# Performance work log

Measured on AMD Instinct MI355X. Metric: run time of the kernel, lower is better.

## Reference

```python
import jax, jax.numpy as jnp
import numpy as np

STEPS = 8  # number of scaling-and-squaring steps


def _identity_grid(D, H, W, dtype):
    # (D, H, W, 3) voxel-coordinate identity transformation
    z = jnp.arange(D, dtype=dtype)
    y = jnp.arange(H, dtype=dtype)
    x = jnp.arange(W, dtype=dtype)
    return jnp.stack(jnp.meshgrid(z, y, x, indexing='ij'), axis=-1)


def _pull_wrap(v, phi):
    """Trilinear sampling of field v at voxel coords phi with circular ('dft') bound.

    v:   (B, D, H, W, 3) vector field (values)
    phi: (B, D, H, W, 3) sampling coordinates in voxel space (z, y, x order)
    """
    B, D, H, W, C = v.shape
    f = jnp.floor(phi)
    w1 = phi - f          # weight of the +1 corner
    w0 = 1.0 - w1
    i0 = f.astype(jnp.int32)
    dims = jnp.array([D, H, W], dtype=jnp.int32)
    i0 = jnp.mod(i0, dims)          # wrap (dft) boundary
    i1 = jnp.mod(i0 + 1, dims)
    zs, ys, xs = (i0[..., 0], i1[..., 0]), (i0[..., 1], i1[..., 1]), (i0[..., 2], i1[..., 2])
    wzs, wys, wxs = (w0[..., 0], w1[..., 0]), (w0[..., 1], w1[..., 1]), (w0[..., 2], w1[..., 2])
    vflat = v.reshape(B, D * H * W, C)
    out = jnp.zeros_like(v)
    for a in range(2):
        for b in range(2):
            for c in range(2):
                lin = (zs[a] * H + ys[b]) * W + xs[c]              # (B, D, H, W)
                vals = jnp.take_along_axis(vflat, lin.reshape(B, -1, 1), axis=1)
                vals = vals.reshape(B, D, H, W, C)
                out = out + (wzs[a] * wys[b] * wxs[c])[..., None] * vals
    return out


def setup_inputs() -> dict:
    key = jax.random.key(0)
    velocity = jax.random.normal(key, (2, 128, 128, 128, 3), dtype=jnp.float32)
    return {"velocity": velocity}


def reference(velocity):
    # Scaling and squaring: v <- v/2^K; repeat K times: v <- v + v o (id + v)
    B, D, H, W, C = velocity.shape
    grid = _identity_grid(D, H, W, velocity.dtype)[None]  # (1, D, H, W, 3)
    v = velocity / (2.0 ** STEPS)
    for _ in range(STEPS):
        v = v + _pull_wrap(v, grid + v)
    # displacement=False -> return transformation field id + displacement
    return grid + v
```

## Files before the change

### kernel.cpp

```cpp
#include <hip/hip_runtime.h>
#include <hip/hip_fp16.h>


#define DHW   (128 * 128 * 128)
#define NVOX  (2 * DHW)
#define RW    129

#if defined(__has_builtin)
#  if __has_builtin(__builtin_amdgcn_global_load_lds)
#    define HAVE_ASYNC 1
#  endif
#endif
#ifndef HAVE_ASYNC
#  define HAVE_ASYNC 0
#endif

#if HAVE_ASYNC
#define ASYNC_DW(lptr, gptr)                                            \
    __builtin_amdgcn_global_load_lds(                                   \
        (__attribute__((address_space(1))) void*)(gptr),                \
        (__attribute__((address_space(3))) void*)(lptr), 4, 0, 0)
#else
#define ASYNC_DW(lptr, gptr)  (*(lptr) = *(gptr))
#endif

__device__ __forceinline__ __half2 bc_h2(unsigned u) {
    return *reinterpret_cast<__half2*>(&u);
}

__device__ __forceinline__ void acc_cell(uint2 c, float w,
                                         float& az, float& ay, float& ax) {
    __half2 c0 = bc_h2(c.x), c1 = bc_h2(c.y);
    az = fmaf(w, __low2float(c0),  az);
    ay = fmaf(w, __high2float(c0), ay);
    ax = fmaf(w, __low2float(c1),  ax);
}

template <bool IN_F32, int H, int BX, int BZ, int NB, bool PAD_OUT>
__global__ __launch_bounds__(512) void sq_sten_async(
    const float* __restrict__ velf,
    const uint2* __restrict__ fin,
    uint2* __restrict__ fout)
{
    constexpr int LBX = (BX == 64) ? 6 : 5;
    constexpr int TX = BX + 2 * H, TY = 8 + 2 * H, TZ = BZ + 2 * H;
    constexpr int TS = TX * TY * TZ;
    constexpr int DWS = TS * 2;
    constexpr int NP  = (DWS + 511) / 512;
    constexpr int PF  = (TS + 511) / 512;
    constexpr int VPT = (BX * BZ) / 64;
    constexpr int NXB = 128 / BX, LNX = 7 - LBX;
    static_assert(2 * TS * 8 <= 64 * 1024, "dbuf exceeds 64KB static LDS");
    static_assert(128 % (BZ * NB) == 0 && 128 / (BZ * NB) == 8, "z grouping");
    __shared__ uint2 lds[2][TS];

    int t = (int)threadIdx.x;
    int b = (int)blockIdx.x;
    int X = (b & (NXB - 1)) << LBX;
    int b2 = b >> LNX;
    int Y = (b2 & 15) << 3;
    int b3 = b2 >> 4;
    int Z0 = (b3 & 7) * (BZ * NB);
    int batch = b3 >> 3;
    int bb21 = batch << 21;

    unsigned sxy[NP];
    unsigned szzp[(NP + 3) / 4];
    if (!IN_F32) {
#pragma unroll
        for (int q = 0; q < (NP + 3) / 4; ++q) szzp[q] = 0;
#pragma unroll
        for (int p = 0; p < NP; ++p) {
            int idx = t + p * 512;
            if (idx < DWS) {
                int cell = idx >> 1, half = idx & 1;
                int xx = cell % TX;
                int rem = cell / TX;
                int yy = rem % TY, zz = rem / TY;
                int gx = (X - H + xx) & 127;
                int gy = (Y - H + yy) & 127;
                sxy[p] = (unsigned)(((((gy << 7) | gx)) << 1) | half);
                szzp[p >> 2] |= (unsigned)zz << ((p & 3) * 8);
            } else {
                sxy[p] = 0;
            }
        }
    }

    const unsigned* fdw = (const unsigned*)fin;

#define STAGE_ASYNC(ZB, BUF)                                            \
    { unsigned* ldw = (unsigned*)(BUF);                                 \
      _Pragma("unroll")                                                 \
      for (int p = 0; p < NP; ++p) {                                    \
          int idx = t + p * 512;                                        \
          if (idx < DWS) {                                              \
              int zz = (int)((szzp[p >> 2] >> ((p & 3) * 8)) & 255u);   \
              int gz = ((ZB) - H + zz) & 127;                           \
              ASYNC_DW(ldw + idx,                                       \
                       fdw + (bb21 << 1) + (gz << 15) + (int)sxy[p]);   \
          }                                                             \
      } }

#define STAGE_F32(ZB, BUF)                                              \
    { _Pragma("unroll")                                                 \
      for (int p = 0; p < PF; ++p) {                                    \
          int idx = t + p * 512;                                        \
          if (idx < TS) {                                               \
              int xx = idx % TX;                                        \
              int rem = idx / TX;                                       \
              int yy = rem % TY, zz = rem / TY;                         \
              int gx = (X - H + xx) & 127;                              \
              int gy = (Y - H + yy) & 127;                              \
              int gz = ((ZB) - H + zz) & 127;                           \
              size_t a = (size_t)((batch << 21) | (gz << 14) |          \
                                  (gy << 7) | gx) * 3;                  \
              const float s = 1.0f / 256.0f;                            \
              __half2 q0 = __floats2half2_rn(velf[a] * s,               \
                                             velf[a + 1] * s);          \
              __half2 q1 = __floats2half2_rn(velf[a + 2] * s, 0.0f);    \
              uint2 cc;                                                 \
              cc.x = *reinterpret_cast<unsigned*>(&q0);                 \
              cc.y = *reinterpret_cast<unsigned*>(&q1);                 \
              (BUF)[idx] = cc;                                          \
          }                                                             \
      } }

    if (IN_F32) { STAGE_F32(Z0, lds[0]) }
    else        { STAGE_ASYNC(Z0, lds[0]) }
    __syncthreads();

    int lx = t & (BX - 1);
    int ly = (t >> LBX) & 7;
    int lz0 = (t >> (LBX + 3)) * VPT;

    for (int i = 0; i < NB; ++i) {
        int Z = Z0 + i * BZ;
        const uint2* tile = IN_F32 ? lds[0] : lds[i & 1];

        if (!IN_F32 && i + 1 < NB) { STAGE_ASYNC(Z + BZ, lds[(i + 1) & 1]) }

        uint2 sd[VPT];
#pragma unroll
        for (int v = 0; v < VPT; ++v) {
            int lz = lz0 + v;
            int cidx = ((lz + H) * TY + (ly + H)) * TX + (lx + H);
            uint2 c = tile[cidx];
            __half2 c0 = bc_h2(c.x), c1 = bc_h2(c.y);
            float vz = __low2float(c0), vy = __high2float(c0), vx = __low2float(c1);

            float pz = (float)(Z + lz) + vz;
            float py = (float)(Y + ly) + vy;
            float px = (float)(X + lx) + vx;
            float fz = floorf(pz), fy = floorf(py), fx = floorf(px);
            float wz1 = pz - fz, wy1 = py - fy, wx1 = px - fx;
            float wz0 = 1.0f - wz1, wy0 = 1.0f - wy1, wx0 = 1.0f - wx1;

            int izl = (int)fz - Z + H;
            int iyl = (int)fy - Y + H;
            int ixl = (int)fx - X + H;

            float wzy00 = wz0 * wy0, wzy01 = wz0 * wy1;
            float wzy10 = wz1 * wy0, wzy11 = wz1 * wy1;

            float az = 0.0f, ay = 0.0f, ax = 0.0f;
            int i00 = (izl * TY + iyl) * TX + ixl;
            int i01 = i00 + TX;
            int i10 = i00 + TY * TX;
            int i11 = i10 + TX;

            acc_cell(tile[i00],     wzy00 * wx0, az, ay, ax);
            acc_cell(tile[i00 + 1], wzy00 * wx1, az, ay, ax);
            acc_cell(tile[i01],     wzy01 * wx0, az, ay, ax);
            acc_cell(tile[i01 + 1], wzy01 * wx1, az, ay, ax);
            acc_cell(tile[i10],     wzy10 * wx0, az, ay, ax);
            acc_cell(tile[i10 + 1], wzy10 * wx1, az, ay, ax);
            acc_cell(tile[i11],     wzy11 * wx0, az, ay, ax);
            acc_cell(tile[i11 + 1], wzy11 * wx1, az, ay, ax);

            __half2 p0 = __floats2half2_rn(vz + az, vy + ay);
            __half2 p1 = __floats2half2_rn(vx + ax, 0.0f);
            sd[v].x = *reinterpret_cast<unsigned*>(&p0);
            sd[v].y = *reinterpret_cast<unsigned*>(&p1);
        }

#pragma unroll
        for (int v = 0; v < VPT; ++v) {
            int lz = lz0 + v;
            int z_ = Z + lz, y_ = Y + ly, x_ = X + lx;
            if (PAD_OUT) {
                int rS = (batch << 14) + (z_ << 7) + y_;
                int pidx = (rS << 7) + rS + x_;
                fout[pidx] = sd[v];
                if (x_ == 0) fout[pidx + 128] = sd[v];
            } else {
                fout[bb21 | (z_ << 14) | (y_ << 7) | x_] = sd[v];
            }
        }

        if (i + 1 < NB) {
            __syncthreads();
            if (IN_F32) { STAGE_F32(Z + BZ, lds[0]) __syncthreads(); }
        }
    }
#undef STAGE_ASYNC
#undef STAGE_F32
}

__device__ __forceinline__ void acc_pair(uint4 g, float wl, float wr,
                                         float& az, float& ay, float& ax) {
    __half2 h0 = bc_h2(g.x);
    __half2 h1 = bc_h2(g.y);
    __half2 h2 = bc_h2(g.z);
    __half2 h3 = bc_h2(g.w);
    az += wl * __low2float(h0)  + wr * __low2float(h2);
    ay += wl * __high2float(h0) + wr * __high2float(h2);
    ax += wl * __low2float(h1)  + wr * __low2float(h3);
}

template <bool IN_F32, bool OUT_F32>
__global__ __launch_bounds__(1024) void sq_step_p(
    const void* __restrict__ vin_, void* __restrict__ vout_)
{
    const float* vinf = (const float*)vin_;
    const uint2* vinh = (const uint2*)vin_;

    int t = (int)threadIdx.x;
    int b = (int)blockIdx.x;
    int x = ((b & 1) << 6) | (t & 63);
    int y = (((b >> 1) & 31) << 2) | ((t >> 6) & 3);
    int z = (((b >> 6) & 31) << 2) | (t >> 8);
    int batch = b >> 11;

    const float s = IN_F32 ? (1.0f / 256.0f) : 1.0f;

    int bbr = batch << 14;
    int r   = bbr + (z << 7) + y;

    float vz, vy, vx;
    if (IN_F32) {
        size_t base = ((size_t)(batch << 21) + (z << 14) + (y << 7) + x) * 3;
        vz = vinf[base + 0] * s;
        vy = vinf[base + 1] * s;
        vx = vinf[base + 2] * s;
    } else {
        uint2 c = vinh[(r << 7) + r + x];
        __half2 c0 = bc_h2(c.x), c1 = bc_h2(c.y);
        vz = __low2float(c0); vy = __high2float(c0); vx = __low2float(c1);
    }

    float pz = (float)z + vz, py = (float)y + vy, px = (float)x + vx;
    float fz = floorf(pz), fy = floorf(py), fx = floorf(px);
    float wz1 = pz - fz, wy1 = py - fy, wx1 = px - fx;
    float wz0 = 1.0f - wz1, wy0 = 1.0f - wy1, wx0 = 1.0f - wx1;

    int iz0 = ((int)fz) & 127, iy0 = ((int)fy) & 127, ix0 = ((int)fx) & 127;
    int iz1 = (iz0 + 1) & 127, iy1 = (iy0 + 1) & 127;

    float wzy00 = wz0 * wy0, wzy01 = wz0 * wy1;
    float wzy10 = wz1 * wy0, wzy11 = wz1 * wy1;

    float az = 0.0f, ay = 0.0f, ax = 0.0f;

    if (IN_F32) {
        int bb  = batch << 21;
        int ix1 = (ix0 + 1) & 127;
        int zo0 = bb + (iz0 << 14), zo1 = bb + (iz1 << 14);
        int yo0 = iy0 << 7, yo1 = iy1 << 7;
#define CORNER(ZO, YO, IX, WW)                                          \
        {                                                               \
            size_t a = (size_t)((ZO) + (YO) + (IX)) * 3;                \
            float w = (WW);                                             \
            az += w * (vinf[a] * s);                                    \
            ay += w * (vinf[a + 1] * s);                                \
            ax += w * (vinf[a + 2] * s);                                \
        }
        CORNER(zo0, yo0, ix0, wzy00 * wx0)
        CORNER(zo0, yo0, ix1, wzy00 * wx1)
        CORNER(zo0, yo1, ix0, wzy01 * wx0)
        CORNER(zo0, yo1, ix1, wzy01 * wx1)
        CORNER(zo1, yo0, ix0, wzy10 * wx0)
        CORNER(zo1, yo0, ix1, wzy10 * wx1)
        CORNER(zo1, yo1, ix0, wzy11 * wx0)
        CORNER(zo1, yo1, ix1, wzy11 * wx1)
#undef CORNER
    } else {
        int r00 = bbr + (iz0 << 7) + iy0;
        int r01 = bbr + (iz0 << 7) + iy1;
        int r10 = bbr + (iz1 << 7) + iy0;
        int r11 = bbr + (iz1 << 7) + iy1;
        uint4 g00 = *(const uint4*)(vinh + (r00 << 7) + r00 + ix0);
        uint4 g01 = *(const uint4*)(vinh + (r01 << 7) + r01 + ix0);
        uint4 g10 = *(const uint4*)(vinh + (r10 << 7) + r10 + ix0);
        uint4 g11 = *(const uint4*)(vinh + (r11 << 7) + r11 + ix0);
        acc_pair(g00, wzy00 * wx0, wzy00 * wx1, az, ay, ax);
        acc_pair(g01, wzy01 * wx0, wzy01 * wx1, az, ay, ax);
        acc_pair(g10, wzy10 * wx0, wzy10 * wx1, az, ay, ax);
        acc_pair(g11, wzy11 * wx0, wzy11 * wx1, az, ay, ax);
    }

    float oz = vz + az;
    float oy = vy + ay;
    float ox = vx + ax;

    if (OUT_F32) {
        float* voutf = (float*)vout_;
        size_t base = ((size_t)(batch << 21) + (z << 14) + (y << 7) + x) * 3;
        voutf[base + 0] = oz + (float)z;
        voutf[base + 1] = oy + (float)y;
        voutf[base + 2] = ox + (float)x;
    } else {
        __half2 p0 = __floats2half2_rn(oz, oy);
        __half2 p1 = __floats2half2_rn(ox, 0.0f);
        uint2 sd;
        sd.x = *reinterpret_cast<unsigned*>(&p0);
        sd.y = *reinterpret_cast<unsigned*>(&p1);
        uint2* vouth = (uint2*)vout_;
        int pidx = (r << 7) + r + x;
        vouth[pidx] = sd;
        if (x == 0) vouth[pidx + 128] = sd;
    }
}

extern "C" void kernel_launch(void* const* d_in, const int* in_sizes, int n_in,
                              void* d_out, int out_size, void* d_ws, size_t ws_size,
                              hipStream_t stream) {
    const float* vel = (const float*)d_in[0];
    float* out = (float*)d_out;

    const size_t UB = (size_t)NVOX * 8;
    const size_t PB = (size_t)2 * 128 * 128 * RW * 8;

    dim3 pblock(512);
    dim3 pgrid1(512);
    dim3 pgrid2(1024);
    dim3 ggrid(NVOX / 1024), gblock(1024);

    if (ws_size >= 2 * UB + PB) {
        uint2* U0 = (uint2*)d_ws;
        uint2* U1 = (uint2*)((char*)d_ws + UB);
        uint2* P  = (uint2*)((char*)d_ws + 2 * UB);

        sq_sten_async<true,  1, 64, 4, 4, false><<<pgrid1, pblock, 0, stream>>>(vel, nullptr, U0);
        sq_sten_async<false, 1, 64, 4, 4, false><<<pgrid1, pblock, 0, stream>>>(nullptr, U0, U1);
        sq_sten_async<false, 1, 64, 4, 4, false><<<pgrid1, pblock, 0, stream>>>(nullptr, U1, U0);
        sq_sten_async<false, 1, 64, 4, 4, false><<<pgrid1, pblock, 0, stream>>>(nullptr, U0, U1);
        sq_sten_async<false, 1, 64, 4, 4, false><<<pgrid1, pblock, 0, stream>>>(nullptr, U1, U0);
        sq_sten_async<false, 1, 64, 4, 4, false><<<pgrid1, pblock, 0, stream>>>(nullptr, U0, U1);
        sq_sten_async<false, 2, 32, 4, 4, true ><<<pgrid2, pblock, 0, stream>>>(nullptr, U1, P);
        sq_step_p<false, true ><<<ggrid, gblock, 0, stream>>>(P, out);
    } else {
        void* ws = d_ws;
        sq_step_p<true,  false><<<ggrid, gblock, 0, stream>>>(vel, ws);
        sq_step_p<false, false><<<ggrid, gblock, 0, stream>>>(ws,  out);
        sq_step_p<false, false><<<ggrid, gblock, 0, stream>>>(out, ws);
        sq_step_p<false, false><<<ggrid, gblock, 0, stream>>>(ws,  out);
        sq_step_p<false, false><<<ggrid, gblock, 0, stream>>>(out, ws);
        sq_step_p<false, false><<<ggrid, gblock, 0, stream>>>(ws,  out);
        sq_step_p<false, false><<<ggrid, gblock, 0, stream>>>(out, ws);
        sq_step_p<false, true ><<<ggrid, gblock, 0, stream>>>(ws,  out);
    }
}
```

Baseline: 276.8 us.

## Unroll brick pipeline with fine-grained vmcnt waits and split first-step kernel

The async stencil kernel is split into a dedicated fp32-input first-step kernel and an fp16 DMA kernel. The DMA kernel's four z-bricks are fully unrolled with two named LDS buffers, and each brick writes its outputs inline instead of buffering them. Per-brick __syncthreads is replaced by an explicit s_waitcnt vmcnt(N) that still lets the last brick's global stores be in flight, plus an lgkmcnt wait, sched barriers and s_barrier. The goal is to stop blocking on outstanding stores at each brick boundary and to remove the template branching. The hand-written vmcnt literal assumes a fixed ordering of memory ops, which is fragile if the compiler reorders them.

```diff
diff --git a/kernel.cpp b/kernel.cpp
--- a/kernel.cpp
+++ b/kernel.cpp
@@ -15,15 +15,6 @@
 #  define HAVE_ASYNC 0
 #endif
 
-#if HAVE_ASYNC
-#define ASYNC_DW(lptr, gptr)                                            \
-    __builtin_amdgcn_global_load_lds(                                   \
-        (__attribute__((address_space(1))) void*)(gptr),                \
-        (__attribute__((address_space(3))) void*)(lptr), 4, 0, 0)
-#else
-#define ASYNC_DW(lptr, gptr)  (*(lptr) = *(gptr))
-#endif
-
 __device__ __forceinline__ __half2 bc_h2(unsigned u) {
     return *reinterpret_cast<__half2*>(&u);
 }
@@ -36,23 +27,22 @@
     ax = fmaf(w, __low2float(c1),  ax);
 }
 
-template <bool IN_F32, int H, int BX, int BZ, int NB, bool PAD_OUT>
-__global__ __launch_bounds__(512) void sq_sten_async(
-    const float* __restrict__ velf,
-    const uint2* __restrict__ fin,
-    uint2* __restrict__ fout)
+template <int H, int BX, int BZ, bool PAD_OUT>
+__global__ __launch_bounds__(512) void sq_sten_dma(
+    const uint2* __restrict__ fin, uint2* __restrict__ fout)
 {
     constexpr int LBX = (BX == 64) ? 6 : 5;
+    constexpr int NB = 4;
     constexpr int TX = BX + 2 * H, TY = 8 + 2 * H, TZ = BZ + 2 * H;
     constexpr int TS = TX * TY * TZ;
     constexpr int DWS = TS * 2;
     constexpr int NP  = (DWS + 511) / 512;
-    constexpr int PF  = (TS + 511) / 512;
     constexpr int VPT = (BX * BZ) / 64;
     constexpr int NXB = 128 / BX, LNX = 7 - LBX;
     static_assert(2 * TS * 8 <= 64 * 1024, "dbuf exceeds 64KB static LDS");
-    static_assert(128 % (BZ * NB) == 0 && 128 / (BZ * NB) == 8, "z grouping");
-    __shared__ uint2 lds[2][TS];
+    static_assert(VPT == 4 || VPT == 2, "vmcnt literal needs 4 or 2");
+    __shared__ uint2 bufA[TS];
+    __shared__ uint2 bufB[TS];
 
     int t = (int)threadIdx.x;
     int b = (int)blockIdx.x;
@@ -66,30 +56,37 @@
 
     unsigned sxy[NP];
     unsigned szzp[(NP + 3) / 4];
-    if (!IN_F32) {
 #pragma unroll
-        for (int q = 0; q < (NP + 3) / 4; ++q) szzp[q] = 0;
+    for (int q = 0; q < (NP + 3) / 4; ++q) szzp[q] = 0;
 #pragma unroll
-        for (int p = 0; p < NP; ++p) {
-            int idx = t + p * 512;
-            if (idx < DWS) {
-                int cell = idx >> 1, half = idx & 1;
-                int xx = cell % TX;
-                int rem = cell / TX;
-                int yy = rem % TY, zz = rem / TY;
-                int gx = (X - H + xx) & 127;
-                int gy = (Y - H + yy) & 127;
-                sxy[p] = (unsigned)(((((gy << 7) | gx)) << 1) | half);
-                szzp[p >> 2] |= (unsigned)zz << ((p & 3) * 8);
-            } else {
-                sxy[p] = 0;
-            }
+    for (int p = 0; p < NP; ++p) {
+        int idx = t + p * 512;
+        if (idx < DWS) {
+            int cell = idx >> 1, half = idx & 1;
+            int xx = cell % TX;
+            int rem = cell / TX;
+            int yy = rem % TY, zz = rem / TY;
+            int gx = (X - H + xx) & 127;
+            int gy = (Y - H + yy) & 127;
+            sxy[p] = (unsigned)((((gy << 7) | gx) << 1) | half);
+            szzp[p >> 2] |= (unsigned)zz << ((p & 3) * 8);
+        } else {
+            sxy[p] = 0;
         }
     }
 
     const unsigned* fdw = (const unsigned*)fin;
 
-#define STAGE_ASYNC(ZB, BUF)                                            \
+#if HAVE_ASYNC
+#define ASYNC_DW(lptr, gptr)                                            \
+    __builtin_amdgcn_global_load_lds(                                   \
+        (const __attribute__((address_space(1))) unsigned*)(gptr),      \
+        (__attribute__((address_space(3))) unsigned*)(lptr), 4, 0, 0)
+#else
+#define ASYNC_DW(lptr, gptr)  (*(lptr) = *(gptr))
+#endif
+
+#define STAGE(ZB, BUF)                                                  \
     { unsigned* ldw = (unsigned*)(BUF);                                 \
       _Pragma("unroll")                                                 \
       for (int p = 0; p < NP; ++p) {                                    \
@@ -100,75 +97,164 @@
               ASYNC_DW(ldw + idx,                                       \
                        fdw + (bb21 << 1) + (gz << 15) + (int)sxy[p]);   \
           }                                                             \
-      } }
-
-#define STAGE_F32(ZB, BUF)                                              \
-    { _Pragma("unroll")                                                 \
-      for (int p = 0; p < PF; ++p) {                                    \
-          int idx = t + p * 512;                                        \
-          if (idx < TS) {                                               \
-              int xx = idx % TX;                                        \
-              int rem = idx / TX;                                       \
-              int yy = rem % TY, zz = rem / TY;                         \
-              int gx = (X - H + xx) & 127;                              \
-              int gy = (Y - H + yy) & 127;                              \
-              int gz = ((ZB) - H + zz) & 127;                           \
-              size_t a = (size_t)((batch << 21) | (gz << 14) |          \
-                                  (gy << 7) | gx) * 3;                  \
-              const float s = 1.0f / 256.0f;                            \
-              __half2 q0 = __floats2half2_rn(velf[a] * s,               \
-                                             velf[a + 1] * s);          \
-              __half2 q1 = __floats2half2_rn(velf[a + 2] * s, 0.0f);    \
-              uint2 cc;                                                 \
-              cc.x = *reinterpret_cast<unsigned*>(&q0);                 \
-              cc.y = *reinterpret_cast<unsigned*>(&q1);                 \
-              (BUF)[idx] = cc;                                          \
-          }                                                             \
-      } }
-
-    if (IN_F32) { STAGE_F32(Z0, lds[0]) }
-    else        { STAGE_ASYNC(Z0, lds[0]) }
-    __syncthreads();
+      }                                                                 \
+      __builtin_amdgcn_sched_barrier(0); }
 
     int lx = t & (BX - 1);
     int ly = (t >> LBX) & 7;
     int lz0 = (t >> (LBX + 3)) * VPT;
 
-    for (int i = 0; i < NB; ++i) {
+#define COMPUTE(TILE, Z)                                                \
+    { _Pragma("unroll")                                                 \
+      for (int v = 0; v < VPT; ++v) {                                   \
+          int lz = lz0 + v;                                             \
+          int cidx = ((lz + H) * TY + (ly + H)) * TX + (lx + H);        \
+          uint2 c = (TILE)[cidx];                                       \
+          __half2 c0 = bc_h2(c.x), c1 = bc_h2(c.y);                     \
+          float vz = __low2float(c0), vy = __high2float(c0);            \
+          float vx = __low2float(c1);                                   \
+          float pz = (float)((Z) + lz) + vz;                            \
+          float py = (float)(Y + ly) + vy;                              \
+          float px = (float)(X + lx) + vx;                              \
+          float fz = floorf(pz), fy = floorf(py), fx = floorf(px);      \
+          float wz1 = pz - fz, wy1 = py - fy, wx1 = px - fx;            \
+          float wz0 = 1.0f - wz1, wy0 = 1.0f - wy1, wx0 = 1.0f - wx1;   \
+          int izl = (int)fz - (Z) + H;                                  \
+          int iyl = (int)fy - Y + H;                                    \
+          int ixl = (int)fx - X + H;                                    \
+          float wzy00 = wz0 * wy0, wzy01 = wz0 * wy1;                   \
+          float wzy10 = wz1 * wy0, wzy11 = wz1 * wy1;                   \
+          float az = 0.0f, ay = 0.0f, ax = 0.0f;                        \
+          int i00 = (izl * TY + iyl) * TX + ixl;                        \
+          int i01 = i00 + TX;                                           \
+          int i10 = i00 + TY * TX;                                      \
+          int i11 = i10 + TX;                                           \
+          acc_cell((TILE)[i00],     wzy00 * wx0, az, ay, ax);           \
+          acc_cell((TILE)[i00 + 1], wzy00 * wx1, az, ay, ax);           \
+          acc_cell((TILE)[i01],     wzy01 * wx0, az, ay, ax);           \
+          acc_cell((TILE)[i01 + 1], wzy01 * wx1, az, ay, ax);           \
+          acc_cell((TILE)[i10],     wzy10 * wx0, az, ay, ax);           \
+          acc_cell((TILE)[i10 + 1], wzy10 * wx1, az, ay, ax);           \
+          acc_cell((TILE)[i11],     wzy11 * wx0, az, ay, ax);           \
+          acc_cell((TILE)[i11 + 1], wzy11 * wx1, az, ay, ax);           \
+          __half2 p0 = __floats2half2_rn(vz + az, vy + ay);             \
+          __half2 p1 = __floats2half2_rn(vx + ax, 0.0f);                \
+          uint2 sd;                                                     \
+          sd.x = *reinterpret_cast<unsigned*>(&p0);                     \
+          sd.y = *reinterpret_cast<unsigned*>(&p1);                     \
+          int z_ = (Z) + lz, y_ = Y + ly, x_ = X + lx;                  \
+          if (PAD_OUT) {                                                \
+              int rS = (batch << 14) + (z_ << 7) + y_;                  \
+              int pidx = (rS << 7) + rS + x_;                           \
+              fout[pidx] = sd;                                          \
+              if (x_ == 0) fout[pidx + 128] = sd;                       \
+          } else {                                                      \
+              fout[bb21 | (z_ << 14) | (y_ << 7) | x_] = sd;            \
+          }                                                             \
+      } }
+
+#if HAVE_ASYNC
+#define BRICK_BAR                                                       \
+    if (VPT == 4) asm volatile("s_waitcnt vmcnt(4)" ::: "memory");      \
+    else          asm volatile("s_waitcnt vmcnt(2)" ::: "memory");      \
+    __builtin_amdgcn_sched_barrier(0);                                  \
+    asm volatile("s_waitcnt lgkmcnt(0)" ::: "memory");                  \
+    __builtin_amdgcn_sched_barrier(0);                                  \
+    __builtin_amdgcn_s_barrier();                                       \
+    __builtin_amdgcn_sched_barrier(0);
+#else
+#define BRICK_BAR __syncthreads();
+#endif
+
+    STAGE(Z0, bufA)
+    __syncthreads();
+
+    STAGE(Z0 + BZ, bufB)
+    COMPUTE(bufA, Z0)
+    BRICK_BAR
+    STAGE(Z0 + 2 * BZ, bufA)
+    COMPUTE(bufB, Z0 + BZ)
+    BRICK_BAR
+    STAGE(Z0 + 3 * BZ, bufB)
+    COMPUTE(bufA, Z0 + 2 * BZ)
+    BRICK_BAR
+    COMPUTE(bufB, Z0 + 3 * BZ)
+
+#undef STAGE
+#undef COMPUTE
+#undef BRICK_BAR
+#undef ASYNC_DW
+}
+
+__global__ __launch_bounds__(512) void sq_step1(
+    const float* __restrict__ velf, uint2* __restrict__ fout)
+{
+    constexpr int H = 1, BX = 64, BZ = 4;
+    constexpr int TX = 66, TY = 10, TZ = 6, TS = TX * TY * TZ;
+    constexpr int PF = (TS + 511) / 512;
+    constexpr int VPT = 4;
+    __shared__ uint2 tile[TS];
+
+    int t = (int)threadIdx.x;
+    int b = (int)blockIdx.x;
+    int X = (b & 1) << 6;
+    int b2 = b >> 1;
+    int Y = (b2 & 15) << 3;
+    int b3 = b2 >> 4;
+    int Z0 = (b3 & 7) << 4;
+    int batch = b3 >> 3;
+    int bb21 = batch << 21;
+
+    int lx = t & 63, ly = (t >> 6) & 7, lz0 = (t >> 9) * VPT;
+
+    for (int i = 0; i < 4; ++i) {
         int Z = Z0 + i * BZ;
-        const uint2* tile = IN_F32 ? lds[0] : lds[i & 1];
-
-        if (!IN_F32 && i + 1 < NB) { STAGE_ASYNC(Z + BZ, lds[(i + 1) & 1]) }
-
-        uint2 sd[VPT];
+#pragma unroll
+        for (int p = 0; p < PF; ++p) {
+            int idx = t + p * 512;
+            if (idx < TS) {
+                int xx = idx % TX;
+                int rem = idx / TX;
+                int yy = rem % TY, zz = rem / TY;
+                int gx = (X - H + xx) & 127;
+                int gy = (Y - H + yy) & 127;
+                int gz = (Z - H + zz) & 127;
+                size_t a = (size_t)(bb21 | (gz << 14) | (gy << 7) | gx) * 3;
+                const float s = 1.0f / 256.0f;
+                __half2 q0 = __floats2half2_rn(velf[a] * s, velf[a + 1] * s);
+                __half2 q1 = __floats2half2_rn(velf[a + 2] * s, 0.0f);
+                uint2 cc;
+                cc.x = *reinterpret_cast<unsigned*>(&q0);
+                cc.y = *reinterpret_cast<unsigned*>(&q1);
+                tile[idx] = cc;
+            }
+        }
+        __syncthreads();
+
 #pragma unroll
         for (int v = 0; v < VPT; ++v) {
             int lz = lz0 + v;
             int cidx = ((lz + H) * TY + (ly + H)) * TX + (lx + H);
             uint2 c = tile[cidx];
             __half2 c0 = bc_h2(c.x), c1 = bc_h2(c.y);
-            float vz = __low2float(c0), vy = __high2float(c0), vx = __low2float(c1);
-
+            float vz = __low2float(c0), vy = __high2float(c0);
+            float vx = __low2float(c1);
             float pz = (float)(Z + lz) + vz;
             float py = (float)(Y + ly) + vy;
             float px = (float)(X + lx) + vx;
             float fz = floorf(pz), fy = floorf(py), fx = floorf(px);
             float wz1 = pz - fz, wy1 = py - fy, wx1 = px - fx;
             float wz0 = 1.0f - wz1, wy0 = 1.0f - wy1, wx0 = 1.0f - wx1;
-
             int izl = (int)fz - Z + H;
             int iyl = (int)fy - Y + H;
             int ixl = (int)fx - X + H;
-
             float wzy00 = wz0 * wy0, wzy01 = wz0 * wy1;
             float wzy10 = wz1 * wy0, wzy11 = wz1 * wy1;
-
             float az = 0.0f, ay = 0.0f, ax = 0.0f;
             int i00 = (izl * TY + iyl) * TX + ixl;
             int i01 = i00 + TX;
             int i10 = i00 + TY * TX;
             int i11 = i10 + TX;
-
             acc_cell(tile[i00],     wzy00 * wx0, az, ay, ax);
             acc_cell(tile[i00 + 1], wzy00 * wx1, az, ay, ax);
             acc_cell(tile[i01],     wzy01 * wx0, az, ay, ax);
@@ -177,34 +263,16 @@
             acc_cell(tile[i10 + 1], wzy10 * wx1, az, ay, ax);
             acc_cell(tile[i11],     wzy11 * wx0, az, ay, ax);
             acc_cell(tile[i11 + 1], wzy11 * wx1, az, ay, ax);
-
             __half2 p0 = __floats2half2_rn(vz + az, vy + ay);
             __half2 p1 = __floats2half2_rn(vx + ax, 0.0f);
-            sd[v].x = *reinterpret_cast<unsigned*>(&p0);
-            sd[v].y = *reinterpret_cast<unsigned*>(&p1);
+            uint2 sd;
+            sd.x = *reinterpret_cast<unsigned*>(&p0);
+            sd.y = *reinterpret_cast<unsigned*>(&p1);
+            int z_ = Z + lz, y_ = Y + ly, x_ = X + lx;
+            fout[bb21 | (z_ << 14) | (y_ << 7) | x_] = sd;
         }
-
-#pragma unroll
-        for (int v = 0; v < VPT; ++v) {
-            int lz = lz0 + v;
-            int z_ = Z + lz, y_ = Y + ly, x_ = X + lx;
-            if (PAD_OUT) {
-                int rS = (batch << 14) + (z_ << 7) + y_;
-                int pidx = (rS << 7) + rS + x_;
-                fout[pidx] = sd[v];
-                if (x_ == 0) fout[pidx + 128] = sd[v];
-            } else {
-                fout[bb21 | (z_ << 14) | (y_ << 7) | x_] = sd[v];
-            }
-        }
-
-        if (i + 1 < NB) {
-            __syncthreads();
-            if (IN_F32) { STAGE_F32(Z + BZ, lds[0]) __syncthreads(); }
-        }
-    }
-#undef STAGE_ASYNC
-#undef STAGE_F32
+        __syncthreads();
+    }
 }
 
 __device__ __forceinline__ void acc_pair(uint4 g, float wl, float wr,
@@ -341,13 +409,13 @@
         uint2* U1 = (uint2*)((char*)d_ws + UB);
         uint2* P  = (uint2*)((char*)d_ws + 2 * UB);
 
-        sq_sten_async<true,  1, 64, 4, 4, false><<<pgrid1, pblock, 0, stream>>>(vel, nullptr, U0);
-        sq_sten_async<false, 1, 64, 4, 4, false><<<pgrid1, pblock, 0, stream>>>(nullptr, U0, U1);
-        sq_sten_async<false, 1, 64, 4, 4, false><<<pgrid1, pblock, 0, stream>>>(nullptr, U1, U0);
-        sq_sten_async<false, 1, 64, 4, 4, false><<<pgrid1, pblock, 0, stream>>>(nullptr, U0, U1);
-        sq_sten_async<false, 1, 64, 4, 4, false><<<pgrid1, pblock, 0, stream>>>(nullptr, U1, U0);
-        sq_sten_async<false, 1, 64, 4, 4, false><<<pgrid1, pblock, 0, stream>>>(nullptr, U0, U1);
-        sq_sten_async<false, 2, 32, 4, 4, true ><<<pgrid2, pblock, 0, stream>>>(nullptr, U1, P);
+        sq_step1<<<pgrid1, pblock, 0, stream>>>(vel, U0);
+        sq_sten_dma<1, 64, 4, false><<<pgrid1, pblock, 0, stream>>>(U0, U1);
+        sq_sten_dma<1, 64, 4, false><<<pgrid1, pblock, 0, stream>>>(U1, U0);
+        sq_sten_dma<1, 64, 4, false><<<pgrid1, pblock, 0, stream>>>(U0, U1);
+        sq_sten_dma<1, 64, 4, false><<<pgrid1, pblock, 0, stream>>>(U1, U0);
+        sq_sten_dma<1, 64, 4, false><<<pgrid1, pblock, 0, stream>>>(U0, U1);
+        sq_sten_dma<2, 32, 4, true ><<<pgrid2, pblock, 0, stream>>>(U1, P);
         sq_step_p<false, true ><<<ggrid, gblock, 0, stream>>>(P, out);
     } else {
         void* ws = d_ws;
```

Result: faster. 269.1 us (-2.8%).
